# Optimization experiments

Measured on AMD Instinct MI355X. Metric: run time of the kernel, lower is better.

## Reference

```python
import math
import jax, jax.numpy as jnp
import numpy as np

B, T, C = 8, 1024, 768
H = 12
D = C // H  # 64


def setup_inputs() -> dict:
    key = jax.random.key(0)
    k1, k2, k3, k4, k5 = jax.random.split(key, 5)
    s = 0.02
    return {
        "x": jax.random.normal(k1, (B, T, C), dtype=jnp.float32),
        "w_qkv": jax.random.normal(k2, (C, 3 * C), dtype=jnp.float32) * s,
        "b_qkv": jax.random.normal(k3, (3 * C,), dtype=jnp.float32) * s,
        "w_proj": jax.random.normal(k4, (C, C), dtype=jnp.float32) * s,
        "b_proj": jax.random.normal(k5, (C,), dtype=jnp.float32) * s,
    }


def reference(x, w_qkv, b_qkv, w_proj, b_proj):
    b, t, c = x.shape
    qkv = x @ w_qkv + b_qkv                      # [B,T,3C]
    q, k, v = jnp.split(qkv, 3, axis=-1)
    # [B,T,C] -> [B,H,T,D]
    q = q.reshape(b, t, H, D).transpose(0, 2, 1, 3)
    k = k.reshape(b, t, H, D).transpose(0, 2, 1, 3)
    v = v.reshape(b, t, H, D).transpose(0, 2, 1, 3)
    scale = 1.0 / math.sqrt(D)
    att = jnp.einsum("bhqd,bhkd->bhqk", q, k) * scale   # [B,H,T,T]
    causal = jnp.tril(jnp.ones((t, t), dtype=bool))
    att = jnp.where(causal, att, -jnp.inf)
    att = jax.nn.softmax(att, axis=-1)
    y = jnp.einsum("bhqk,bhkd->bhqd", att, v)            # [B,H,T,D]
    y = y.transpose(0, 2, 1, 3).reshape(b, t, c)
    return y @ w_proj + b_proj
```

## Files before the change

kernel.cpp:

```cpp
#include <hip/hip_runtime.h>
#include <math.h>

#define B_ 8
#define T_ 1024
#define C_ 768
#define H_ 12
#define D_ 64

typedef __bf16 bf16x8 __attribute__((ext_vector_type(8)));
typedef float  f32x4  __attribute__((ext_vector_type(4)));
typedef unsigned short us8 __attribute__((ext_vector_type(8)));
typedef unsigned int   u32x4v __attribute__((ext_vector_type(4)));

typedef __attribute__((address_space(3))) void lds_void;
typedef __attribute__((address_space(1))) const void glb_void;

#define KSC 0.18033688011112043f

__device__ __forceinline__ unsigned short f2bf(float f) {
    unsigned int u = __float_as_uint(f);
    u += 0x7fffu + ((u >> 16) & 1u);
    return (unsigned short)(u >> 16);
}

__global__ __launch_bounds__(256)
void prep_w(const float* __restrict__ w_qkv, const float* __restrict__ b_qkv,
            const float* __restrict__ w_proj,
            unsigned short* __restrict__ wqT, unsigned short* __restrict__ wpT,
            float* __restrict__ bqs) {
    __shared__ unsigned short Ts[64][65];
    const int id  = blockIdx.x;
    const int tid = threadIdx.x;
    if (id == 576) {
        for (int i = tid; i < 3 * C_; i += 256)
            bqs[i] = b_qkv[i] * (i < C_ ? KSC : 1.f);
        return;
    }
    const float* W; unsigned short* Wt; int N, nlim, t2;
    if (id < 432) { t2 = id;       W = w_qkv;  Wt = wqT; N = 3 * C_; nlim = C_; }
    else          { t2 = id - 432; W = w_proj; Wt = wpT; N = C_;     nlim = 0;  }
    const int ntiles = N / 64;
    const int n0 = (t2 % ntiles) * 64, k0 = (t2 / ntiles) * 64;
    for (int i = tid; i < 4096; i += 256) {
        int n = i & 63, k = i >> 6;
        float sc = (n0 + n < nlim) ? KSC : 1.f;
        Ts[n][k] = f2bf(W[(size_t)(k0 + k) * N + n0 + n] * sc);
    }
    __syncthreads();
    for (int i = tid; i < 4096; i += 256) {
        int k = i & 63, n = i >> 6;
        Wt[(size_t)(n0 + n) * 768 + k0 + k] = Ts[n][k];
    }
}

template<int A_FP32, int OUT_BF16>
__global__ __launch_bounds__(256, 3)
void gemm_pipe(const float* __restrict__ Af, const unsigned short* __restrict__ A16,
               const unsigned short* __restrict__ Bt, const float* __restrict__ bias,
               void* __restrict__ Cout, int M, int N, int K) {
    __shared__ __align__(16) unsigned short As[8192];
    __shared__ __align__(16) unsigned short Bs[2][8192];

    const int tid  = threadIdx.x;
    const int lane = tid & 63;
    const int c    = lane & 15;
    const int quad = lane >> 4;
    const int wave = tid >> 6;
    const int wm   = (wave >> 1) * 64;
    const int wn   = (wave & 1) * 64;
    const int bm   = blockIdx.x * 128;
    const int bn   = blockIdx.y * 128;

    const float*          aF[4];
    const unsigned short* aH[4];
    int wAddr[4];
#pragma unroll
    for (int p = 0; p < 4; p++) {
        const int Lp = p * 256 + tid;
        const int r  = Lp >> 3;
        const int kc = (Lp ^ r) & 7;
        if (A_FP32) aF[p] = Af  + (size_t)(bm + r) * K + kc * 8;
        else        aH[p] = A16 + (size_t)(bm + r) * K + kc * 8;
        wAddr[p] = Lp * 8;
    }
    const unsigned short* bS[4];
#pragma unroll
    for (int p = 0; p < 4; p++) {
        const int Lp = p * 256 + tid;
        const int L  = Lp ^ ((Lp >> 3) & 7);
        bS[p] = Bt + (size_t)(bn + (L >> 3)) * K + (L & 7) * 8;
    }
    const int wb = (tid & 0xC0) * 8;

    int aoff[4][2], boff[4][2];
#pragma unroll
    for (int i = 0; i < 4; i++)
#pragma unroll
        for (int ks = 0; ks < 2; ks++) {
            const int kcA = (ks * 4 + quad) ^ (c & 7);
            aoff[i][ks] = ((wm + i * 16 + c) * 8 + kcA) * 8;
            boff[i][ks] = ((wn + i * 16 + c) * 8 + kcA) * 8;
        }

    float4 a0[4], a1[4];
    us8    aR[4];
    f32x4 acc[4][4];
#pragma unroll
    for (int i = 0; i < 4; i++)
#pragma unroll
        for (int j = 0; j < 4; j++) acc[i][j] = (f32x4){0.f, 0.f, 0.f, 0.f};

#pragma unroll
    for (int p = 0; p < 4; p++) {
        __builtin_amdgcn_global_load_lds((glb_void*)bS[p],
            (lds_void*)(&Bs[0][0] + p * 2048 + wb), 16, 0, 0);
        bS[p] += 64;
        if (A_FP32) { a0[p] = *(const float4*)aF[p]; a1[p] = *(const float4*)(aF[p] + 4); aF[p] += 64; }
        else        { aR[p] = *(const us8*)aH[p]; aH[p] += 64; }
    }

    const int R = K >> 6;
    for (int r = 0; r < R; r++) {
        __syncthreads();
#pragma unroll
        for (int p = 0; p < 4; p++) {
            us8 w;
            if (A_FP32) {
                w[0] = f2bf(a0[p].x); w[1] = f2bf(a0[p].y);
                w[2] = f2bf(a0[p].z); w[3] = f2bf(a0[p].w);
                w[4] = f2bf(a1[p].x); w[5] = f2bf(a1[p].y);
                w[6] = f2bf(a1[p].z); w[7] = f2bf(a1[p].w);
            } else w = aR[p];
            *(us8*)&As[wAddr[p]] = w;
        }
        __syncthreads();

        if (r + 1 < R) {
#pragma unroll
            for (int p = 0; p < 4; p++) {
                __builtin_amdgcn_global_load_lds((glb_void*)bS[p],
                    (lds_void*)(&Bs[(r + 1) & 1][0] + p * 2048 + wb), 16, 0, 0);
                bS[p] += 64;
                if (A_FP32) { a0[p] = *(const float4*)aF[p]; a1[p] = *(const float4*)(aF[p] + 4); aF[p] += 64; }
                else        { aR[p] = *(const us8*)aH[p]; aH[p] += 64; }
            }
        }

        const unsigned short* bbuf = &Bs[r & 1][0];
#pragma unroll
        for (int ks = 0; ks < 2; ks++) {
            bf16x8 af[4], bfr[4];
#pragma unroll
            for (int i = 0; i < 4; i++)
                af[i] = __builtin_bit_cast(bf16x8, *(const us8*)&As[aoff[i][ks]]);
#pragma unroll
            for (int j = 0; j < 4; j++)
                bfr[j] = __builtin_bit_cast(bf16x8, *(const us8*)&bbuf[boff[j][ks]]);
#pragma unroll
            for (int i = 0; i < 4; i++)
#pragma unroll
                for (int j = 0; j < 4; j++)
                    acc[i][j] = __builtin_amdgcn_mfma_f32_16x16x32_bf16(af[i], bfr[j], acc[i][j], 0, 0, 0);
        }
    }

    float bs[4];
#pragma unroll
    for (int j = 0; j < 4; j++) bs[j] = bias[bn + wn + j * 16 + c];
#pragma unroll
    for (int i = 0; i < 4; i++) {
        const int gm = bm + wm + i * 16 + quad * 4;
#pragma unroll
        for (int r = 0; r < 4; r++) {
            const size_t ro = (size_t)(gm + r) * N;
#pragma unroll
            for (int j = 0; j < 4; j++) {
                const float v = acc[i][j][r] + bs[j];
                const int gn = bn + wn + j * 16 + c;
                if (OUT_BF16) ((unsigned short*)Cout)[ro + gn] = f2bf(v);
                else          ((float*)Cout)[ro + gn] = v;
            }
        }
    }
}

__device__ __forceinline__ int sigmaK(int k) {
    return 16 * (2 * (k >> 5) + ((k >> 2) & 1)) + 4 * ((k >> 3) & 3) + (k & 3);
}

__global__ __launch_bounds__(256, 3)
void attn_mfma(const unsigned short* __restrict__ qkv, unsigned short* __restrict__ y) {
    __shared__ __align__(16) unsigned short Ks[64 * 72];
    __shared__ __align__(16) unsigned int   Vt[64 * 36];

    const int tid  = threadIdx.x;
    const int wave = tid >> 6;
    const int lane = tid & 63;
    const int c    = lane & 15;
    const int quad = lane >> 4;

    const int id = blockIdx.x;
    const int p  = (id >> 3) & 7;
    const int bh = (id >> 6) * 8 + (id & 7);
    const int b  = bh / H_;
    const int h  = bh - b * H_;

    const int qts[2] = {p, 15 - p};
    const int q0s[2] = {p * 64, (15 - p) * 64};

    const int RS = 3 * C_;
    const unsigned short* kbase = qkv + (size_t)b * T_ * RS + C_ + h * D_;
    const unsigned short* vbase = qkv + (size_t)b * T_ * RS + 2 * C_ + h * D_;

    const u32x4v onesu = {0x3F803F80u, 0x3F803F80u, 0x3F803F80u, 0x3F803F80u};
    const bf16x8 onesf = __builtin_bit_cast(bf16x8, onesu);

    bf16x8 qf[2][2];
#pragma unroll
    for (int t = 0; t < 2; t++) {
        const unsigned short* qrow =
            qkv + ((size_t)(b * T_ + q0s[t] + wave * 16 + c)) * RS + h * D_ + quad * 8;
        qf[t][0] = __builtin_bit_cast(bf16x8, *(const us8*)qrow);
        qf[t][1] = __builtin_bit_cast(bf16x8, *(const us8*)(qrow + 32));
    }

    const int kr0 = tid >> 3, kc0 = tid & 7;
    const int sK0 = sigmaK(kr0) * 72 + kc0 * 8;
    const int sK1 = sigmaK(kr0 + 32) * 72 + kc0 * 8;
    const int dg  = tid >> 4, kp0 = tid & 15;

    us8 kA, kB;
    ushort4 vA0, vB0, vA1, vB1;
    {
        kA = *(const us8*)(kbase + (size_t)kr0 * RS + kc0 * 8);
        kB = *(const us8*)(kbase + (size_t)(kr0 + 32) * RS + kc0 * 8);
        const unsigned short* p0 = vbase + (size_t)(2 * kp0) * RS + dg * 4;
        vA0 = *(const ushort4*)p0;  vB0 = *(const ushort4*)(p0 + RS);
        const unsigned short* p1 = vbase + (size_t)(2 * (kp0 + 16)) * RS + dg * 4;
        vA1 = *(const ushort4*)p1;  vB1 = *(const ushort4*)(p1 + RS);
    }

    f32x4 Oa[2][4];
    f32x4 Ol[2];
#pragma unroll
    for (int t = 0; t < 2; t++) {
        Ol[t] = (f32x4){0.f, 0.f, 0.f, 0.f};
#pragma unroll
        for (int d = 0; d < 4; d++) Oa[t][d] = (f32x4){0.f, 0.f, 0.f, 0.f};
    }

    const int ktEnd = qts[1];
    for (int kt = 0; kt <= ktEnd; kt++) {
        __syncthreads();
        *(us8*)&Ks[sK0] = kA;
        *(us8*)&Ks[sK1] = kB;
        {
            unsigned int* v0 = &Vt[(dg * 4) * 36 + kp0];
            v0[0]   = vA0.x | ((unsigned)vB0.x << 16);
            v0[36]  = vA0.y | ((unsigned)vB0.y << 16);
            v0[72]  = vA0.z | ((unsigned)vB0.z << 16);
            v0[108] = vA0.w | ((unsigned)vB0.w << 16);
            unsigned int* v1 = v0 + 16;
            v1[0]   = vA1.x | ((unsigned)vB1.x << 16);
            v1[36]  = vA1.y | ((unsigned)vB1.y << 16);
            v1[72]  = vA1.z | ((unsigned)vB1.z << 16);
            v1[108] = vA1.w | ((unsigned)vB1.w << 16);
        }
        __syncthreads();

        if (kt < ktEnd) {
            const unsigned short* kp = kbase + (size_t)((kt + 1) * 64) * RS;
            kA = *(const us8*)(kp + (size_t)kr0 * RS + kc0 * 8);
            kB = *(const us8*)(kp + (size_t)(kr0 + 32) * RS + kc0 * 8);
            const unsigned short* vp = vbase + (size_t)((kt + 1) * 64) * RS;
            const unsigned short* p0 = vp + (size_t)(2 * kp0) * RS + dg * 4;
            vA0 = *(const ushort4*)p0;  vB0 = *(const ushort4*)(p0 + RS);
            const unsigned short* p1 = vp + (size_t)(2 * (kp0 + 16)) * RS + dg * 4;
            vA1 = *(const ushort4*)p1;  vB1 = *(const ushort4*)(p1 + RS);
        }

        bf16x8 kf[4][2];
#pragma unroll
        for (int nb = 0; nb < 4; nb++) {
#pragma unroll
            for (int ks = 0; ks < 2; ks++)
                kf[nb][ks] = __builtin_bit_cast(bf16x8,
                    *(const us8*)&Ks[(nb * 16 + c) * 72 + quad * 8 + ks * 32]);
        }

#pragma unroll
        for (int t = 0; t < 2; t++) {
            if (kt > qts[t]) continue;
            const bool diag = (kt == qts[t]);
            const bool doHi = !diag || (wave >= 2);
            const int nbmax = diag ? ((wave >= 2) ? 3 : 1) : 3;

            f32x4 sv[4];
#pragma unroll
            for (int nb = 0; nb < 4; nb++) {
                if (nb <= nbmax) {
                    f32x4 z = (f32x4){0.f, 0.f, 0.f, 0.f};
                    z = __builtin_amdgcn_mfma_f32_16x16x32_bf16(kf[nb][0], qf[t][0], z, 0, 0, 0);
                    sv[nb] = __builtin_amdgcn_mfma_f32_16x16x32_bf16(kf[nb][1], qf[t][1], z, 0, 0, 0);
                }
            }
            if (diag) {
                const int qloc = wave * 16 + c;
#pragma unroll
                for (int nb = 0; nb < 4; nb++) {
                    if (nb <= nbmax) {
                        const int kb = 32 * (nb >> 1) + 4 * (nb & 1) + 8 * quad;
#pragma unroll
                        for (int r = 0; r < 4; r++)
                            if (kb + r > qloc) sv[nb][r] = -INFINITY;
                    }
                }
            }

            unsigned int pd[4][2];
#pragma unroll
            for (int nb = 0; nb < 4; nb++) {
                if (nb <= nbmax) {
                    float p0 = __builtin_amdgcn_exp2f(sv[nb][0]);
                    float p1 = __builtin_amdgcn_exp2f(sv[nb][1]);
                    float p2 = __builtin_amdgcn_exp2f(sv[nb][2]);
                    float p3 = __builtin_amdgcn_exp2f(sv[nb][3]);
                    unsigned u0 = __float_as_uint(p0) + 0x8000u;
                    unsigned u1 = __float_as_uint(p1) + 0x8000u;
                    unsigned u2 = __float_as_uint(p2) + 0x8000u;
                    unsigned u3 = __float_as_uint(p3) + 0x8000u;
                    pd[nb][0] = (u0 >> 16) | (u1 & 0xffff0000u);
                    pd[nb][1] = (u2 >> 16) | (u3 & 0xffff0000u);
                } else {
                    pd[nb][0] = 0u; pd[nb][1] = 0u;
                }
            }

            bf16x8 ap0 = __builtin_bit_cast(bf16x8,
                (u32x4v){pd[0][0], pd[0][1], pd[1][0], pd[1][1]});
            bf16x8 ap1 = __builtin_bit_cast(bf16x8,
                (u32x4v){pd[2][0], pd[2][1], pd[3][0], pd[3][1]});

            Ol[t] = __builtin_amdgcn_mfma_f32_16x16x32_bf16(ap0, onesf, Ol[t], 0, 0, 0);
            if (doHi)
                Ol[t] = __builtin_amdgcn_mfma_f32_16x16x32_bf16(ap1, onesf, Ol[t], 0, 0, 0);

#pragma unroll
            for (int dd = 0; dd < 4; dd++) {
                const unsigned int* vrow = &Vt[(dd * 16 + c) * 36 + quad * 4];
                bf16x8 vb0 = __builtin_bit_cast(bf16x8, *(const u32x4v*)vrow);
                Oa[t][dd] = __builtin_amdgcn_mfma_f32_16x16x32_bf16(ap0, vb0, Oa[t][dd], 0, 0, 0);
                if (doHi) {
                    bf16x8 vb1 = __builtin_bit_cast(bf16x8, *(const u32x4v*)(vrow + 16));
                    Oa[t][dd] = __builtin_amdgcn_mfma_f32_16x16x32_bf16(ap1, vb1, Oa[t][dd], 0, 0, 0);
                }
            }
        }
    }

#pragma unroll
    for (int t = 0; t < 2; t++) {
        unsigned short* yrow =
            y + ((size_t)(b * T_ + q0s[t] + wave * 16)) * C_ + h * D_;
#pragma unroll
        for (int r = 0; r < 4; r++) {
            float inv = 1.f / Ol[t][r];
#pragma unroll
            for (int dd = 0; dd < 4; dd++)
                yrow[(size_t)(quad * 4 + r) * C_ + dd * 16 + c] = f2bf(Oa[t][dd][r] * inv);
        }
    }
}

extern "C" void kernel_launch(void* const* d_in, const int* in_sizes, int n_in,
                              void* d_out, int out_size, void* d_ws, size_t ws_size,
                              hipStream_t stream) {
    const float* x      = (const float*)d_in[0];
    const float* w_qkv  = (const float*)d_in[1];
    const float* b_qkv  = (const float*)d_in[2];
    const float* w_proj = (const float*)d_in[3];
    const float* b_proj = (const float*)d_in[4];
    float* out = (float*)d_out;

    unsigned short* wqT  = (unsigned short*)d_ws;
    unsigned short* wpT  = wqT  + (size_t)3 * C_ * C_;
    unsigned short* qkvb = wpT  + (size_t)C_ * C_;
    unsigned short* yb   = qkvb + (size_t)B_ * T_ * 3 * C_;
    float*          bqs  = (float*)(yb + (size_t)B_ * T_ * C_);

    prep_w<<<577, 256, 0, stream>>>(w_qkv, b_qkv, w_proj, wqT, wpT, bqs);

    gemm_pipe<1, 1><<<dim3(B_ * T_ / 128, 3 * C_ / 128), 256, 0, stream>>>(
        x, nullptr, wqT, bqs, qkvb, B_ * T_, 3 * C_, C_);

    attn_mfma<<<8 * B_ * H_, 256, 0, stream>>>(qkvb, yb);

    gemm_pipe<0, 0><<<dim3(B_ * T_ / 128, C_ / 128), 256, 0, stream>>>(
        nullptr, yb, wpT, b_proj, out, B_ * T_, C_, C_);
}
```

Baseline: 183.3 us.

## Double-buffer A tile, shrink K-step to 32, and use 64-row tiles for projection GEMM

The GEMM now double-buffers the A tile in LDS as well as B, so it needs one barrier per K-step instead of two. The K-step drops from 64 to 32 to shrink LDS and raise occupancy (launch bounds go from 3 to 4 blocks), and the swizzle is adapted to 4 chunks per row. A template tile height lets the output projection use 64-row tiles, doubling its grid for better CU fill. The trade-off is twice as many loop iterations with less MFMA work per barrier.

```diff
diff --git a/kernel.cpp b/kernel.cpp
--- a/kernel.cpp
+++ b/kernel.cpp
@@ -53,114 +53,130 @@
     }
 }
 
-template<int A_FP32, int OUT_BF16>
-__global__ __launch_bounds__(256, 3)
+template<int TM, int A_FP32, int OUT_BF16>
+__global__ __launch_bounds__(256, 4)
 void gemm_pipe(const float* __restrict__ Af, const unsigned short* __restrict__ A16,
                const unsigned short* __restrict__ Bt, const float* __restrict__ bias,
                void* __restrict__ Cout, int M, int N, int K) {
-    __shared__ __align__(16) unsigned short As[8192];
-    __shared__ __align__(16) unsigned short Bs[2][8192];
+    const int PA = TM / 64;
+    const int MI = TM / 32;
+    __shared__ __align__(16) unsigned short As[2][TM * 32];
+    __shared__ __align__(16) unsigned short Bs[2][4096];
 
     const int tid  = threadIdx.x;
     const int lane = tid & 63;
     const int c    = lane & 15;
     const int quad = lane >> 4;
     const int wave = tid >> 6;
-    const int wm   = (wave >> 1) * 64;
+    const int wm   = (wave >> 1) * (TM / 2);
     const int wn   = (wave & 1) * 64;
-    const int bm   = blockIdx.x * 128;
+    const int bm   = blockIdx.x * TM;
     const int bn   = blockIdx.y * 128;
 
-    const float*          aF[4];
-    const unsigned short* aH[4];
-    int wAddr[4];
-#pragma unroll
-    for (int p = 0; p < 4; p++) {
+    const float*          aF[PA];
+    const unsigned short* aH[PA];
+    int wAddr[PA];
+#pragma unroll
+    for (int p = 0; p < PA; p++) {
         const int Lp = p * 256 + tid;
-        const int r  = Lp >> 3;
-        const int kc = (Lp ^ r) & 7;
+        const int r  = Lp >> 2;
+        const int kc = (Lp ^ r) & 3;
         if (A_FP32) aF[p] = Af  + (size_t)(bm + r) * K + kc * 8;
         else        aH[p] = A16 + (size_t)(bm + r) * K + kc * 8;
         wAddr[p] = Lp * 8;
     }
-    const unsigned short* bS[4];
-#pragma unroll
-    for (int p = 0; p < 4; p++) {
+    const unsigned short* bS[2];
+#pragma unroll
+    for (int p = 0; p < 2; p++) {
         const int Lp = p * 256 + tid;
-        const int L  = Lp ^ ((Lp >> 3) & 7);
-        bS[p] = Bt + (size_t)(bn + (L >> 3)) * K + (L & 7) * 8;
+        const int r  = Lp >> 2;
+        const int kc = (Lp ^ r) & 3;
+        bS[p] = Bt + (size_t)(bn + r) * K + kc * 8;
     }
     const int wb = (tid & 0xC0) * 8;
 
-    int aoff[4][2], boff[4][2];
-#pragma unroll
-    for (int i = 0; i < 4; i++)
-#pragma unroll
-        for (int ks = 0; ks < 2; ks++) {
-            const int kcA = (ks * 4 + quad) ^ (c & 7);
-            aoff[i][ks] = ((wm + i * 16 + c) * 8 + kcA) * 8;
-            boff[i][ks] = ((wn + i * 16 + c) * 8 + kcA) * 8;
-        }
-
-    float4 a0[4], a1[4];
-    us8    aR[4];
-    f32x4 acc[4][4];
-#pragma unroll
-    for (int i = 0; i < 4; i++)
+    int aoff[MI], boff[4];
+#pragma unroll
+    for (int i = 0; i < MI; i++)
+        aoff[i] = ((wm + i * 16 + c) * 4 + (quad ^ (c & 3))) * 8;
+#pragma unroll
+    for (int j = 0; j < 4; j++)
+        boff[j] = ((wn + j * 16 + c) * 4 + (quad ^ (c & 3))) * 8;
+
+    float4 a0[PA], a1[PA];
+    us8    aR[PA];
+    f32x4 acc[MI][4];
+#pragma unroll
+    for (int i = 0; i < MI; i++)
 #pragma unroll
         for (int j = 0; j < 4; j++) acc[i][j] = (f32x4){0.f, 0.f, 0.f, 0.f};
 
 #pragma unroll
-    for (int p = 0; p < 4; p++) {
+    for (int p = 0; p < PA; p++) {
+        if (A_FP32) { a0[p] = *(const float4*)aF[p]; a1[p] = *(const float4*)(aF[p] + 4); aF[p] += 32; }
+        else        { aR[p] = *(const us8*)aH[p]; aH[p] += 32; }
+    }
+#pragma unroll
+    for (int p = 0; p < 2; p++) {
         __builtin_amdgcn_global_load_lds((glb_void*)bS[p],
             (lds_void*)(&Bs[0][0] + p * 2048 + wb), 16, 0, 0);
-        bS[p] += 64;
-        if (A_FP32) { a0[p] = *(const float4*)aF[p]; a1[p] = *(const float4*)(aF[p] + 4); aF[p] += 64; }
-        else        { aR[p] = *(const us8*)aH[p]; aH[p] += 64; }
-    }
-
-    const int R = K >> 6;
+        bS[p] += 32;
+    }
+#pragma unroll
+    for (int p = 0; p < PA; p++) {
+        us8 w;
+        if (A_FP32) {
+            w[0] = f2bf(a0[p].x); w[1] = f2bf(a0[p].y);
+            w[2] = f2bf(a0[p].z); w[3] = f2bf(a0[p].w);
+            w[4] = f2bf(a1[p].x); w[5] = f2bf(a1[p].y);
+            w[6] = f2bf(a1[p].z); w[7] = f2bf(a1[p].w);
+        } else w = aR[p];
+        *(us8*)&As[0][wAddr[p]] = w;
+    }
+
+    const int R = K >> 5;
     for (int r = 0; r < R; r++) {
         __syncthreads();
-#pragma unroll
-        for (int p = 0; p < 4; p++) {
-            us8 w;
-            if (A_FP32) {
-                w[0] = f2bf(a0[p].x); w[1] = f2bf(a0[p].y);
-                w[2] = f2bf(a0[p].z); w[3] = f2bf(a0[p].w);
-                w[4] = f2bf(a1[p].x); w[5] = f2bf(a1[p].y);
-                w[6] = f2bf(a1[p].z); w[7] = f2bf(a1[p].w);
-            } else w = aR[p];
-            *(us8*)&As[wAddr[p]] = w;
-        }
-        __syncthreads();
-
+        const int bb = r & 1, nb = bb ^ 1;
         if (r + 1 < R) {
 #pragma unroll
-            for (int p = 0; p < 4; p++) {
+            for (int p = 0; p < PA; p++) {
+                if (A_FP32) { a0[p] = *(const float4*)aF[p]; a1[p] = *(const float4*)(aF[p] + 4); aF[p] += 32; }
+                else        { aR[p] = *(const us8*)aH[p]; aH[p] += 32; }
+            }
+#pragma unroll
+            for (int p = 0; p < 2; p++) {
                 __builtin_amdgcn_global_load_lds((glb_void*)bS[p],
-                    (lds_void*)(&Bs[(r + 1) & 1][0] + p * 2048 + wb), 16, 0, 0);
-                bS[p] += 64;
-                if (A_FP32) { a0[p] = *(const float4*)aF[p]; a1[p] = *(const float4*)(aF[p] + 4); aF[p] += 64; }
-                else        { aR[p] = *(const us8*)aH[p]; aH[p] += 64; }
-            }
-        }
-
-        const unsigned short* bbuf = &Bs[r & 1][0];
-#pragma unroll
-        for (int ks = 0; ks < 2; ks++) {
-            bf16x8 af[4], bfr[4];
-#pragma unroll
-            for (int i = 0; i < 4; i++)
-                af[i] = __builtin_bit_cast(bf16x8, *(const us8*)&As[aoff[i][ks]]);
+                    (lds_void*)(&Bs[nb][0] + p * 2048 + wb), 16, 0, 0);
+                bS[p] += 32;
+            }
+        }
+
+        bf16x8 af[MI], bfr[4];
+#pragma unroll
+        for (int i = 0; i < MI; i++)
+            af[i] = __builtin_bit_cast(bf16x8, *(const us8*)&As[bb][aoff[i]]);
+#pragma unroll
+        for (int j = 0; j < 4; j++)
+            bfr[j] = __builtin_bit_cast(bf16x8, *(const us8*)&Bs[bb][boff[j]]);
+#pragma unroll
+        for (int i = 0; i < MI; i++)
 #pragma unroll
             for (int j = 0; j < 4; j++)
-                bfr[j] = __builtin_bit_cast(bf16x8, *(const us8*)&bbuf[boff[j][ks]]);
-#pragma unroll
-            for (int i = 0; i < 4; i++)
-#pragma unroll
-                for (int j = 0; j < 4; j++)
-                    acc[i][j] = __builtin_amdgcn_mfma_f32_16x16x32_bf16(af[i], bfr[j], acc[i][j], 0, 0, 0);
+                acc[i][j] = __builtin_amdgcn_mfma_f32_16x16x32_bf16(af[i], bfr[j], acc[i][j], 0, 0, 0);
+
+        if (r + 1 < R) {
+#pragma unroll
+            for (int p = 0; p < PA; p++) {
+                us8 w;
+                if (A_FP32) {
+                    w[0] = f2bf(a0[p].x); w[1] = f2bf(a0[p].y);
+                    w[2] = f2bf(a0[p].z); w[3] = f2bf(a0[p].w);
+                    w[4] = f2bf(a1[p].x); w[5] = f2bf(a1[p].y);
+                    w[6] = f2bf(a1[p].z); w[7] = f2bf(a1[p].w);
+                } else w = aR[p];
+                *(us8*)&As[nb][wAddr[p]] = w;
+            }
         }
     }
 
@@ -168,7 +184,7 @@
 #pragma unroll
     for (int j = 0; j < 4; j++) bs[j] = bias[bn + wn + j * 16 + c];
 #pragma unroll
-    for (int i = 0; i < 4; i++) {
+    for (int i = 0; i < MI; i++) {
         const int gm = bm + wm + i * 16 + quad * 4;
 #pragma unroll
         for (int r = 0; r < 4; r++) {
@@ -390,11 +406,11 @@
 
     prep_w<<<577, 256, 0, stream>>>(w_qkv, b_qkv, w_proj, wqT, wpT, bqs);
 
-    gemm_pipe<1, 1><<<dim3(B_ * T_ / 128, 3 * C_ / 128), 256, 0, stream>>>(
+    gemm_pipe<128, 1, 1><<<dim3(B_ * T_ / 128, 3 * C_ / 128), 256, 0, stream>>>(
         x, nullptr, wqT, bqs, qkvb, B_ * T_, 3 * C_, C_);
 
     attn_mfma<<<8 * B_ * H_, 256, 0, stream>>>(qkvb, yb);
 
-    gemm_pipe<0, 0><<<dim3(B_ * T_ / 128, C_ / 128), 256, 0, stream>>>(
+    gemm_pipe<64, 0, 0><<<dim3(B_ * T_ / 64, C_ / 128), 256, 0, stream>>>(
         nullptr, yb, wpT, b_proj, out, B_ * T_, C_, C_);
 }
```

New measurement: 191.2 us. +4.3%, slower.
